# Kernel tuning notes

Hardware: AMD Instinct MI355X
Metric: run time of the kernel (lower is better)

## Reference

```python
import jax, jax.numpy as jnp
import numpy as np

BITS = 4
QMAX = (1 << BITS) - 1      # 15
QHALF = 1 << (BITS - 1)     # 8
B, S = 4, 2048
IN, OUT, FP = 4096, 4096, 256
INT = IN - FP


def setup_inputs() -> dict:
    key = jax.random.key(0)
    k0, k1, k2, k3 = jax.random.split(key, 4)
    x = jax.random.normal(k0, (B, S, IN), dtype=jnp.float16)
    # disjoint outlier / int feature index sets (QUIK splits columns by outlier-ness)
    perm = np.random.default_rng(0).permutation(IN)
    fp_indices = jnp.sort(jnp.asarray(perm[:FP], dtype=jnp.int32))
    int_indices = jnp.sort(jnp.asarray(perm[FP:], dtype=jnp.int32))
    # unpacked int4 weight values in [-8, 7] (torch stores these packed 2-per-uint8)
    int_weight = jax.random.randint(k1, (OUT, INT), -QHALF, QHALF, dtype=jnp.int8)
    weights_scales = (jax.random.uniform(k2, (OUT, 1), dtype=jnp.float32) * 0.01 + 1e-3).astype(jnp.float16)
    fp_weight = (jax.random.normal(k3, (OUT, FP), dtype=jnp.float32) * 0.02).astype(jnp.float16)
    bias = jnp.zeros((OUT,), dtype=jnp.float16)
    # reduced_w[j] = w_scale[j] * sum_k int_weight[j, k]  (precomputed zero-point correction)
    reduced_w = (weights_scales.astype(jnp.float32)[:, 0] * jnp.sum(int_weight.astype(jnp.float32), axis=1)).reshape(1, OUT).astype(jnp.float16)
    return {"x": x, "int_weight": int_weight, "fp_weight": fp_weight, "bias": bias,
            "weights_scales": weights_scales, "reduced_w": reduced_w,
            "int_indices": int_indices, "fp_indices": fp_indices}


def reference(x, int_weight, fp_weight, bias, weights_scales, reduced_w, int_indices, fp_indices):
    b, s, in_feat = x.shape
    xf = x.reshape(-1, in_feat)                       # [N, in] tokens
    int_x = xf[:, int_indices].astype(jnp.float32)    # [N, INT]
    fp_x = xf[:, fp_indices].astype(jnp.float32)      # [N, FP] outliers stay fp16-precision
    # asymmetric per-token quantization (quik.asymmetric.quantize)
    mn = jnp.min(int_x, axis=1, keepdims=True)
    mx = jnp.max(int_x, axis=1, keepdims=True)
    scale = jnp.maximum((mx - mn) / QMAX, 1e-8)       # [N,1]
    q = (jnp.clip(jnp.round((int_x - mn) / scale), 0, QMAX) - QHALF).astype(jnp.int8)  # signed int4 in [-8,7]
    zero = scale * QHALF + mn                         # [N,1] shifted zero point
    # int4 GEMM (quik.matmul.int4Matmul), int32 accumulate
    int_res = jnp.einsum('nk,ok->no', q, int_weight, preferred_element_type=jnp.int32)
    # fp outlier branch fused with bias (F.linear)
    fp_res = fp_x @ fp_weight.astype(jnp.float32).T + bias.astype(jnp.float32)[None, :]
    # quik.asymmetric.dequantize: q*scale_x*scale_w + zero_x*reduced_w + fp_result
    out = (int_res.astype(jnp.float32) * scale * weights_scales.astype(jnp.float32)[:, 0][None, :]
           + zero * reduced_w.astype(jnp.float32) + fp_res)
    return out.astype(jnp.float16).reshape(b, s, -1)
```

## Files before the change

### kernel.cpp

```cpp
#include <hip/hip_runtime.h>
#include <hip/hip_bf16.h>
#include <stdint.h>

#define N_TOK 8192
#define IN_F  4096
#define OUT_F 4096
#define FP_F  256
#define INT_F 3840

typedef int    v4i   __attribute__((ext_vector_type(4)));
typedef int    v16i  __attribute__((ext_vector_type(16)));
typedef float  v16f  __attribute__((ext_vector_type(16)));
typedef __bf16 bf16x8 __attribute__((ext_vector_type(8)));

#define WS_QP   0u
#define WS_WP   31457280u
#define WS_FPX  47185920u
#define WS_WFP  51380224u
#define WS_F1   53477376u
#define WS_F2   53510144u
#define WS_F3   53542912u
#define WS_NEED 53575680u


__global__ __launch_bounds__(256) void zero_out_kernel(uint4* __restrict__ o) {
  o[(size_t)blockIdx.x * 256 + threadIdx.x] = uint4{0, 0, 0, 0};
}

__global__ __launch_bounds__(256, 4) void prep_kernel(
    const float* __restrict__ x,
    const int* __restrict__ int_idx, const int* __restrict__ fp_idx,
    const int* __restrict__ int_w, const float* __restrict__ fp_w,
    uint8_t* __restrict__ qp, uint8_t* __restrict__ wp,
    __hip_bfloat16* __restrict__ fpx, __hip_bfloat16* __restrict__ wfp,
    float* __restrict__ f1, float* __restrict__ f2, float* __restrict__ f3) {
  int tid = threadIdx.x;
  int blk = blockIdx.x;

  if (blk >= 2048) {
    int pb = blk - 2048;
    if (pb < 15360) {
      int t = pb * 256 + tid;
      int r = t / 960, u = t % 960;
      const int* src = int_w + (size_t)r * INT_F + u * 4;
      int4 w4 = *(const int4*)src;
      uint32_t pk = (uint32_t)((w4.x + 8) & 15) |
                    (uint32_t)((w4.y + 8) & 15) << 8 |
                    (uint32_t)((w4.z + 8) & 15) << 16 |
                    (uint32_t)((w4.w + 8) & 15) << 24;
      int g = u >> 2;
      int gp = (g & ~3) | ((g & 3) ^ ((r >> 1) & 3));
      ((uint32_t*)wp)[(size_t)r * 960 + gp * 4 + (u & 3)] = pk;
    } else {
      int t = (pb - 15360) * 256 + tid;
      int i = t * 4;
      int r = i >> 8, c = i & 255;
      float4 v = *(const float4*)(fp_w + i);
      __hip_bfloat16 b[4] = {__float2bfloat16(v.x), __float2bfloat16(v.y),
                             __float2bfloat16(v.z), __float2bfloat16(v.w)};
      int cs = (c & ~0x18) | (((((c) >> 3) & 3) ^ ((r >> 1) & 3)) << 3);
      *(uint2*)(wfp + (size_t)r * 256 + cs) = *(const uint2*)b;
    }
    return;
  }

  int wave = tid >> 6, l = tid & 63;
  int n = blk * 4 + wave;
  const float* xr = x + (size_t)n * IN_F;

  float v[60];
  float lmn = 1e30f, lmx = -1e30f;
#pragma unroll
  for (int k = 0; k < 15; k++) {
    int4 id = *(const int4*)&int_idx[4 * l + 256 * k];
    v[4 * k + 0] = xr[id.x]; v[4 * k + 1] = xr[id.y];
    v[4 * k + 2] = xr[id.z]; v[4 * k + 3] = xr[id.w];
#pragma unroll
    for (int j = 0; j < 4; j++) {
      lmn = fminf(lmn, v[4 * k + j]);
      lmx = fmaxf(lmx, v[4 * k + j]);
    }
  }
  {
    int sw2 = (n >> 1) & 3;
#pragma unroll
    for (int j = 0; j < 4; j++) {
      int c = l + 64 * j;
      int cs = (c & ~0x18) | ((((c >> 3) & 3) ^ sw2) << 3);
      fpx[(size_t)n * FP_F + cs] = __float2bfloat16(xr[fp_idx[c]]);
    }
  }

#pragma unroll
  for (int off = 32; off > 0; off >>= 1) {
    lmn = fminf(lmn, __shfl_xor(lmn, off, 64));
    lmx = fmaxf(lmx, __shfl_xor(lmx, off, 64));
  }
  float mn = lmn;
  float sc = fmaxf((lmx - mn) / 15.0f, 1e-8f);
  float inv = 1.0f / sc;
  if (l == 0) { f1[n] = sc; f3[n] = mn; }

  int sw4 = (n >> 1) & 3;
  uint32_t* qrow = (uint32_t*)(qp + (size_t)n * INT_F);
  float lsum = 0.0f;
#pragma unroll
  for (int k = 0; k < 15; k++) {
    uint32_t pk = 0;
#pragma unroll
    for (int j = 0; j < 4; j++) {
      float c = fminf(fmaxf(rintf((v[4 * k + j] - mn) * inv), 0.0f), 15.0f);
      lsum += c;
      pk |= (uint32_t)c << (8 * j);
    }
    int g = (l >> 2) + 16 * k;
    int gp = (g & ~3) | ((g & 3) ^ sw4);
    qrow[gp * 4 + (l & 3)] = pk;
  }
#pragma unroll
  for (int off = 32; off > 0; off >>= 1) lsum += __shfl_xor(lsum, off, 64);
  if (l == 0) f2[n] = -8.0f * lsum * sc;
}

__device__ __forceinline__ void gl16(const void* g, void* l) {
  __builtin_amdgcn_global_load_lds(
      (const __attribute__((address_space(1))) void*)g,
      (__attribute__((address_space(3))) void*)l, 16, 0, 0);
}

__global__ __launch_bounds__(512, 2) void gemm_kernel(
    const uint8_t* __restrict__ qp, const uint8_t* __restrict__ wp,
    const __hip_bfloat16* __restrict__ fpx, const __hip_bfloat16* __restrict__ wfp,
    const float* __restrict__ f1, const float* __restrict__ f2,
    const float* __restrict__ f3,
    const float* __restrict__ wscale, const float* __restrict__ reduced,
    const float* __restrict__ bias, float* __restrict__ out) {
  __shared__ int4 lds4[6144];
  int8_t* lds = (int8_t*)lds4;

  int tid = threadIdx.x;
  int wave = tid >> 6, lane = tid & 63;
  int wm = wave >> 2, wn = wave & 3;
  int blk = blockIdx.x;
  int wg = (blk & 7) * 64 + (blk >> 3);
  int tileM = wg & 31, tileN = wg >> 5;
  int n0 = tileM * 256, o0 = tileN * 256;

  union { v16i i; v16f f; } acc[4][2];
#pragma unroll
  for (int mi = 0; mi < 4; mi++)
#pragma unroll
    for (int ni = 0; ni < 2; ni++)
#pragma unroll
      for (int e = 0; e < 16; e++) acc[mi][ni].i[e] = 0;

  int m = lane & 31, kg = lane >> 5;

  int row0 = tid >> 2, q16b = (tid & 3) * 16;
  int l0 = tid * 16;
  const uint8_t* gA0 = qp + (size_t)(n0 + row0) * INT_F + q16b;
  const uint8_t* gA1 = qp + (size_t)(n0 + 128 + row0) * INT_F + q16b;
  const uint8_t* gB0 = wp + (size_t)(o0 + row0) * INT_F + q16b;
  const uint8_t* gB1 = wp + (size_t)(o0 + 128 + row0) * INT_F + q16b;

#define STAGE_A(base, kt) do {                                   \
    gl16(gA0 + (kt) * 64, lds + (base) + l0);                    \
    gl16(gA1 + (kt) * 64, lds + (base) + 8192 + l0);             \
  } while (0)
#define STAGE_B(base, kt) do {                                   \
    gl16(gB0 + (kt) * 64, lds + (base) + 16384 + l0);            \
    gl16(gB1 + (kt) * 64, lds + (base) + 24576 + l0);            \
  } while (0)

  STAGE_A(0, 0); STAGE_B(0, 0);
  STAGE_A(32768, 1); STAGE_B(32768, 1);
  asm volatile("s_waitcnt vmcnt(4)" ::: "memory");
  __builtin_amdgcn_s_barrier();

#pragma unroll 1
  for (int t = 0; t < 60; t++) {
    int rb = (t % 3) * 32768;
    int sb = ((t + 2) % 3) * 32768;
    bool st = (t + 2 < 60);
#pragma unroll
    for (int ks = 0; ks < 2; ks++) {
      int s = ks * 2 + kg;
      v4i a[4], b[2];
#pragma unroll
      for (int mi = 0; mi < 4; mi++) {
        int row = wm * 128 + mi * 32 + m;
        a[mi] = *(const v4i*)&lds[rb + row * 64 + ((s ^ ((row >> 1) & 3)) * 16)];
      }
#pragma unroll
      for (int ni = 0; ni < 2; ni++) {
        int row = wn * 64 + ni * 32 + m;
        b[ni] = *(const v4i*)&lds[rb + 16384 + row * 64 + ((s ^ ((row >> 1) & 3)) * 16)];
      }
      if (st) { if (ks == 0) STAGE_A(sb, t + 2); else STAGE_B(sb, t + 2); }
      __builtin_amdgcn_s_barrier();
      asm volatile("s_waitcnt lgkmcnt(0)" ::: "memory");
      __builtin_amdgcn_sched_barrier(0);
      __builtin_amdgcn_s_setprio(1);
#pragma unroll
      for (int mi = 0; mi < 4; mi++)
#pragma unroll
        for (int ni = 0; ni < 2; ni++)
          acc[mi][ni].i = __builtin_amdgcn_mfma_i32_32x32x32_i8(
              a[mi], b[ni], acc[mi][ni].i, 0, 0, 0);
      __builtin_amdgcn_s_setprio(0);
      if (ks == 1) {
        if (t < 58) asm volatile("s_waitcnt vmcnt(4)" ::: "memory");
        else        asm volatile("s_waitcnt vmcnt(0)" ::: "memory");
      }
      __builtin_amdgcn_s_barrier();
    }
  }

  const uint8_t* fxb = (const uint8_t*)fpx;
  const uint8_t* fwb = (const uint8_t*)wfp;
  const uint8_t* gFA0 = fxb + (size_t)(n0 + row0) * 512 + q16b;
  const uint8_t* gFA1 = fxb + (size_t)(n0 + 128 + row0) * 512 + q16b;
  const uint8_t* gFB0 = fwb + (size_t)(o0 + row0) * 512 + q16b;
  const uint8_t* gFB1 = fwb + (size_t)(o0 + 128 + row0) * 512 + q16b;

#define STAGE_FA(base, kr) do {                                  \
    gl16(gFA0 + (kr) * 64, lds + (base) + l0);                   \
    gl16(gFA1 + (kr) * 64, lds + (base) + 8192 + l0);            \
  } while (0)
#define STAGE_FB(base, kr) do {                                  \
    gl16(gFB0 + (kr) * 64, lds + (base) + 16384 + l0);           \
    gl16(gFB1 + (kr) * 64, lds + (base) + 24576 + l0);           \
  } while (0)

  STAGE_FA(0, 0); STAGE_FB(0, 0);

  int col = lane & 31, rb4 = (lane >> 5) * 4;
  float cws[2], crw[2], cbs[2];
#pragma unroll
  for (int ni = 0; ni < 2; ni++) {
    int o = o0 + wn * 64 + ni * 32 + col;
    cws[ni] = wscale[o]; crw[ni] = reduced[o]; cbs[ni] = bias[o];
  }
#pragma unroll
  for (int mi = 0; mi < 4; mi++) {
#pragma unroll
    for (int reg = 0; reg < 16; reg++) {
      int row = (reg & 3) + 8 * (reg >> 2) + rb4;
      int n = n0 + wm * 128 + mi * 32 + row;
      float a1 = f1[n], a2 = f2[n], a3 = f3[n];
      float d0 = (float)acc[mi][0].i[reg];
      float d1 = (float)acc[mi][1].i[reg];
      acc[mi][0].f[reg] = (d0 * a1 + a2) * cws[0] + a3 * crw[0] + cbs[0];
      acc[mi][1].f[reg] = (d1 * a1 + a2) * cws[1] + a3 * crw[1] + cbs[1];
    }
  }
  STAGE_FA(32768, 1); STAGE_FB(32768, 1);
  __builtin_amdgcn_s_barrier();

#pragma unroll 1
  for (int r = 0; r < 8; r++) {
    int rb = (r % 3) * 32768;
    int sb = ((r + 2) % 3) * 32768;
    bool st = (r + 2 < 8);
#pragma unroll
    for (int u = 0; u < 2; u++) {
      int s = u * 2 + kg;
      bf16x8 a[4], b[2];
#pragma unroll
      for (int mi = 0; mi < 4; mi++) {
        int row = wm * 128 + mi * 32 + m;
        a[mi] = *(const bf16x8*)&lds[rb + row * 64 + ((s ^ ((row >> 1) & 3)) * 16)];
      }
#pragma unroll
      for (int ni = 0; ni < 2; ni++) {
        int row = wn * 64 + ni * 32 + m;
        b[ni] = *(const bf16x8*)&lds[rb + 16384 + row * 64 + ((s ^ ((row >> 1) & 3)) * 16)];
      }
      if (st) { if (u == 0) STAGE_FA(sb, r + 2); else STAGE_FB(sb, r + 2); }
      __builtin_amdgcn_s_barrier();
      asm volatile("s_waitcnt lgkmcnt(0)" ::: "memory");
      __builtin_amdgcn_sched_barrier(0);
      __builtin_amdgcn_s_setprio(1);
#pragma unroll
      for (int mi = 0; mi < 4; mi++)
#pragma unroll
        for (int ni = 0; ni < 2; ni++)
          acc[mi][ni].f = __builtin_amdgcn_mfma_f32_32x32x16_bf16(
              a[mi], b[ni], acc[mi][ni].f, 0, 0, 0);
      __builtin_amdgcn_s_setprio(0);
      if (u == 1) {
        if (r < 6) asm volatile("s_waitcnt vmcnt(4)" ::: "memory");
        else       asm volatile("s_waitcnt vmcnt(0)" ::: "memory");
      }
      __builtin_amdgcn_s_barrier();
    }
  }
#undef STAGE_A
#undef STAGE_B
#undef STAGE_FA
#undef STAGE_FB

#pragma unroll
  for (int mi = 0; mi < 4; mi++) {
#pragma unroll
    for (int ni = 0; ni < 2; ni++) {
      int o = o0 + wn * 64 + ni * 32 + col;
#pragma unroll
      for (int reg = 0; reg < 16; reg++) {
        int row = (reg & 3) + 8 * (reg >> 2) + rb4;
        int n = n0 + wm * 128 + mi * 32 + row;
        out[(size_t)n * OUT_F + o] = acc[mi][ni].f[reg];
      }
    }
  }
}

extern "C" void kernel_launch(void* const* d_in, const int* in_sizes, int n_in,
                              void* d_out, int out_size, void* d_ws, size_t ws_size,
                              hipStream_t stream) {
  const float* x     = (const float*)d_in[0];
  const int*   int_w = (const int*)d_in[1];
  const float* fp_w  = (const float*)d_in[2];
  const float* bias  = (const float*)d_in[3];
  const float* wsc   = (const float*)d_in[4];
  const float* red   = (const float*)d_in[5];
  const int*   iidx  = (const int*)d_in[6];
  const int*   fidx  = (const int*)d_in[7];
  float*       out   = (float*)d_out;

  if (ws_size < (size_t)WS_NEED) {
    zero_out_kernel<<<out_size / 1024, 256, 0, stream>>>((uint4*)d_out);
    return;
  }

  uint8_t* ws = (uint8_t*)d_ws;
  uint8_t*        qp  = ws + WS_QP;
  uint8_t*        wpk = ws + WS_WP;
  __hip_bfloat16* fpx = (__hip_bfloat16*)(ws + WS_FPX);
  __hip_bfloat16* wfp = (__hip_bfloat16*)(ws + WS_WFP);
  float*          f1  = (float*)(ws + WS_F1);
  float*          f2  = (float*)(ws + WS_F2);
  float*          f3  = (float*)(ws + WS_F3);

  prep_kernel<<<2048 + 15360 + 1024, 256, 0, stream>>>(
      x, iidx, fidx, int_w, fp_w, qp, wpk, fpx, wfp, f1, f2, f3);
  gemm_kernel<<<(N_TOK / 256) * (OUT_F / 256), 512, 0, stream>>>(
      qp, wpk, fpx, wfp, f1, f2, f3, wsc, red, bias, out);
}
```

Measured before the change: 441.3 us.

## Drop LDS staging; load MFMA fragments directly from k-major packed layout

The prep kernel now writes quantized activations, packed weights and the bf16 outlier operands in a k-slab-major layout, so each wave can fetch its MFMA operand fragments straight from global memory with 16-byte coalesced loads. The GEMM drops shared memory, barriers and global_load_lds staging. It uses 128x128 tiles with 4 waves per block and a three-deep register rotation for software pipelining. This removes LDS traffic and synchronisation, but each wave now re-reads A and B fragments through L2 with no intra-block sharing, and the smaller tiles raise total global traffic.

```diff
diff --git a/kernel.cpp b/kernel.cpp
--- a/kernel.cpp
+++ b/kernel.cpp
@@ -48,9 +48,7 @@
                     (uint32_t)((w4.y + 8) & 15) << 8 |
                     (uint32_t)((w4.z + 8) & 15) << 16 |
                     (uint32_t)((w4.w + 8) & 15) << 24;
-      int g = u >> 2;
-      int gp = (g & ~3) | ((g & 3) ^ ((r >> 1) & 3));
-      ((uint32_t*)wp)[(size_t)r * 960 + gp * 4 + (u & 3)] = pk;
+      *(uint32_t*)(wp + (size_t)(u >> 2) * 65536 + (size_t)r * 16 + (u & 3) * 4) = pk;
     } else {
       int t = (pb - 15360) * 256 + tid;
       int i = t * 4;
@@ -58,8 +56,8 @@
       float4 v = *(const float4*)(fp_w + i);
       __hip_bfloat16 b[4] = {__float2bfloat16(v.x), __float2bfloat16(v.y),
                              __float2bfloat16(v.z), __float2bfloat16(v.w)};
-      int cs = (c & ~0x18) | (((((c) >> 3) & 3) ^ ((r >> 1) & 3)) << 3);
-      *(uint2*)(wfp + (size_t)r * 256 + cs) = *(const uint2*)b;
+      *(uint2*)((uint8_t*)wfp + (size_t)(c >> 3) * 65536 + (size_t)r * 16 + (c & 7) * 2) =
+          *(const uint2*)b;
     }
     return;
   }
@@ -82,13 +80,11 @@
     }
   }
   {
-    int sw2 = (n >> 1) & 3;
-#pragma unroll
-    for (int j = 0; j < 4; j++) {
-      int c = l + 64 * j;
-      int cs = (c & ~0x18) | ((((c >> 3) & 3) ^ sw2) << 3);
-      fpx[(size_t)n * FP_F + cs] = __float2bfloat16(xr[fp_idx[c]]);
-    }
+    int4 fid = *(const int4*)&fp_idx[4 * l];
+    __hip_bfloat16 b[4] = {__float2bfloat16(xr[fid.x]), __float2bfloat16(xr[fid.y]),
+                           __float2bfloat16(xr[fid.z]), __float2bfloat16(xr[fid.w])};
+    *(uint2*)((uint8_t*)fpx + (size_t)(l >> 1) * 131072 + (size_t)n * 16 + (l & 1) * 8) =
+        *(const uint2*)b;
   }
 
 #pragma unroll
@@ -101,8 +97,7 @@
   float inv = 1.0f / sc;
   if (l == 0) { f1[n] = sc; f3[n] = mn; }
 
-  int sw4 = (n >> 1) & 3;
-  uint32_t* qrow = (uint32_t*)(qp + (size_t)n * INT_F);
+  uint8_t* qdst = qp + (size_t)(l >> 2) * 131072 + (size_t)n * 16 + (l & 3) * 4;
   float lsum = 0.0f;
 #pragma unroll
   for (int k = 0; k < 15; k++) {
@@ -113,42 +108,31 @@
       lsum += c;
       pk |= (uint32_t)c << (8 * j);
     }
-    int g = (l >> 2) + 16 * k;
-    int gp = (g & ~3) | ((g & 3) ^ sw4);
-    qrow[gp * 4 + (l & 3)] = pk;
+    *(uint32_t*)(qdst + (size_t)k * 2097152) = pk;
   }
 #pragma unroll
   for (int off = 32; off > 0; off >>= 1) lsum += __shfl_xor(lsum, off, 64);
   if (l == 0) f2[n] = -8.0f * lsum * sc;
 }
 
-__device__ __forceinline__ void gl16(const void* g, void* l) {
-  __builtin_amdgcn_global_load_lds(
-      (const __attribute__((address_space(1))) void*)g,
-      (__attribute__((address_space(3))) void*)l, 16, 0, 0);
-}
-
-__global__ __launch_bounds__(512, 2) void gemm_kernel(
+__global__ __launch_bounds__(256, 3) void gemm_kernel(
     const uint8_t* __restrict__ qp, const uint8_t* __restrict__ wp,
     const __hip_bfloat16* __restrict__ fpx, const __hip_bfloat16* __restrict__ wfp,
     const float* __restrict__ f1, const float* __restrict__ f2,
     const float* __restrict__ f3,
     const float* __restrict__ wscale, const float* __restrict__ reduced,
     const float* __restrict__ bias, float* __restrict__ out) {
-  __shared__ int4 lds4[6144];
-  int8_t* lds = (int8_t*)lds4;
-
   int tid = threadIdx.x;
   int wave = tid >> 6, lane = tid & 63;
-  int wm = wave >> 2, wn = wave & 3;
+  int wm = wave >> 1, wn = wave & 1;
   int blk = blockIdx.x;
-  int wg = (blk & 7) * 64 + (blk >> 3);
-  int tileM = wg & 31, tileN = wg >> 5;
-  int n0 = tileM * 256, o0 = tileN * 256;
-
-  union { v16i i; v16f f; } acc[4][2];
-#pragma unroll
-  for (int mi = 0; mi < 4; mi++)
+  int tileM = ((blk & 7) << 3) | ((blk >> 3) & 7);
+  int tileN = blk >> 6;
+  int n0 = tileM * 128, o0 = tileN * 128;
+
+  union { v16i i; v16f f; } acc[2][2];
+#pragma unroll
+  for (int mi = 0; mi < 2; mi++)
 #pragma unroll
     for (int ni = 0; ni < 2; ni++)
 #pragma unroll
@@ -156,83 +140,56 @@
 
   int m = lane & 31, kg = lane >> 5;
 
-  int row0 = tid >> 2, q16b = (tid & 3) * 16;
-  int l0 = tid * 16;
-  const uint8_t* gA0 = qp + (size_t)(n0 + row0) * INT_F + q16b;
-  const uint8_t* gA1 = qp + (size_t)(n0 + 128 + row0) * INT_F + q16b;
-  const uint8_t* gB0 = wp + (size_t)(o0 + row0) * INT_F + q16b;
-  const uint8_t* gB1 = wp + (size_t)(o0 + 128 + row0) * INT_F + q16b;
-
-#define STAGE_A(base, kt) do {                                   \
-    gl16(gA0 + (kt) * 64, lds + (base) + l0);                    \
-    gl16(gA1 + (kt) * 64, lds + (base) + 8192 + l0);             \
-  } while (0)
-#define STAGE_B(base, kt) do {                                   \
-    gl16(gB0 + (kt) * 64, lds + (base) + 16384 + l0);            \
-    gl16(gB1 + (kt) * 64, lds + (base) + 24576 + l0);            \
-  } while (0)
-
-  STAGE_A(0, 0); STAGE_B(0, 0);
-  STAGE_A(32768, 1); STAGE_B(32768, 1);
-  asm volatile("s_waitcnt vmcnt(4)" ::: "memory");
-  __builtin_amdgcn_s_barrier();
-
+  int offA = kg * 131072 + (n0 + wm * 64 + m) * 16;
+  int offB = kg * 65536  + (o0 + wn * 64 + m) * 16;
+
+#define LOADI(S, s) do {                                          \
+    const uint8_t* pa_ = qp + (size_t)(s) * 262144;               \
+    const uint8_t* pb_ = wp + (size_t)(s) * 131072;               \
+    a0##S = *(const v4i*)(pa_ + offA);                            \
+    a1##S = *(const v4i*)(pa_ + offA + 512);                      \
+    b0##S = *(const v4i*)(pb_ + offB);                            \
+    b1##S = *(const v4i*)(pb_ + offB + 512);                      \
+  } while (0)
+#define MFMAI(S) do {                                                         \
+    acc[0][0].i = __builtin_amdgcn_mfma_i32_32x32x32_i8(a0##S, b0##S, acc[0][0].i, 0, 0, 0); \
+    acc[0][1].i = __builtin_amdgcn_mfma_i32_32x32x32_i8(a0##S, b1##S, acc[0][1].i, 0, 0, 0); \
+    acc[1][0].i = __builtin_amdgcn_mfma_i32_32x32x32_i8(a1##S, b0##S, acc[1][0].i, 0, 0, 0); \
+    acc[1][1].i = __builtin_amdgcn_mfma_i32_32x32x32_i8(a1##S, b1##S, acc[1][1].i, 0, 0, 0); \
+  } while (0)
+
+  {
+    v4i a0A, a1A, b0A, b1A, a0B, a1B, b0B, b1B, a0C, a1C, b0C, b1C;
+    LOADI(A, 0); LOADI(B, 1); LOADI(C, 2);
 #pragma unroll 1
-  for (int t = 0; t < 60; t++) {
-    int rb = (t % 3) * 32768;
-    int sb = ((t + 2) % 3) * 32768;
-    bool st = (t + 2 < 60);
-#pragma unroll
-    for (int ks = 0; ks < 2; ks++) {
-      int s = ks * 2 + kg;
-      v4i a[4], b[2];
-#pragma unroll
-      for (int mi = 0; mi < 4; mi++) {
-        int row = wm * 128 + mi * 32 + m;
-        a[mi] = *(const v4i*)&lds[rb + row * 64 + ((s ^ ((row >> 1) & 3)) * 16)];
-      }
-#pragma unroll
-      for (int ni = 0; ni < 2; ni++) {
-        int row = wn * 64 + ni * 32 + m;
-        b[ni] = *(const v4i*)&lds[rb + 16384 + row * 64 + ((s ^ ((row >> 1) & 3)) * 16)];
-      }
-      if (st) { if (ks == 0) STAGE_A(sb, t + 2); else STAGE_B(sb, t + 2); }
-      __builtin_amdgcn_s_barrier();
-      asm volatile("s_waitcnt lgkmcnt(0)" ::: "memory");
-      __builtin_amdgcn_sched_barrier(0);
-      __builtin_amdgcn_s_setprio(1);
-#pragma unroll
-      for (int mi = 0; mi < 4; mi++)
-#pragma unroll
-        for (int ni = 0; ni < 2; ni++)
-          acc[mi][ni].i = __builtin_amdgcn_mfma_i32_32x32x32_i8(
-              a[mi], b[ni], acc[mi][ni].i, 0, 0, 0);
-      __builtin_amdgcn_s_setprio(0);
-      if (ks == 1) {
-        if (t < 58) asm volatile("s_waitcnt vmcnt(4)" ::: "memory");
-        else        asm volatile("s_waitcnt vmcnt(0)" ::: "memory");
-      }
-      __builtin_amdgcn_s_barrier();
-    }
-  }
+    for (int s = 0; s < 117; s += 3) {
+      MFMAI(A); LOADI(A, s + 3);
+      MFMAI(B); LOADI(B, s + 4);
+      MFMAI(C); LOADI(C, s + 5);
+    }
+    MFMAI(A); MFMAI(B); MFMAI(C);
+  }
+#undef LOADI
 
   const uint8_t* fxb = (const uint8_t*)fpx;
   const uint8_t* fwb = (const uint8_t*)wfp;
-  const uint8_t* gFA0 = fxb + (size_t)(n0 + row0) * 512 + q16b;
-  const uint8_t* gFA1 = fxb + (size_t)(n0 + 128 + row0) * 512 + q16b;
-  const uint8_t* gFB0 = fwb + (size_t)(o0 + row0) * 512 + q16b;
-  const uint8_t* gFB1 = fwb + (size_t)(o0 + 128 + row0) * 512 + q16b;
-
-#define STAGE_FA(base, kr) do {                                  \
-    gl16(gFA0 + (kr) * 64, lds + (base) + l0);                   \
-    gl16(gFA1 + (kr) * 64, lds + (base) + 8192 + l0);            \
-  } while (0)
-#define STAGE_FB(base, kr) do {                                  \
-    gl16(gFB0 + (kr) * 64, lds + (base) + 16384 + l0);           \
-    gl16(gFB1 + (kr) * 64, lds + (base) + 24576 + l0);           \
-  } while (0)
-
-  STAGE_FA(0, 0); STAGE_FB(0, 0);
+#define LOADF(S, s) do {                                          \
+    const uint8_t* pa_ = fxb + (size_t)(s) * 262144;              \
+    const uint8_t* pb_ = fwb + (size_t)(s) * 131072;              \
+    fa0##S = *(const bf16x8*)(pa_ + offA);                        \
+    fa1##S = *(const bf16x8*)(pa_ + offA + 512);                  \
+    fb0##S = *(const bf16x8*)(pb_ + offB);                        \
+    fb1##S = *(const bf16x8*)(pb_ + offB + 512);                  \
+  } while (0)
+#define MFMAF(S) do {                                                         \
+    acc[0][0].f = __builtin_amdgcn_mfma_f32_32x32x16_bf16(fa0##S, fb0##S, acc[0][0].f, 0, 0, 0); \
+    acc[0][1].f = __builtin_amdgcn_mfma_f32_32x32x16_bf16(fa0##S, fb1##S, acc[0][1].f, 0, 0, 0); \
+    acc[1][0].f = __builtin_amdgcn_mfma_f32_32x32x16_bf16(fa1##S, fb0##S, acc[1][0].f, 0, 0, 0); \
+    acc[1][1].f = __builtin_amdgcn_mfma_f32_32x32x16_bf16(fa1##S, fb1##S, acc[1][1].f, 0, 0, 0); \
+  } while (0)
+
+  bf16x8 fa0A, fa1A, fb0A, fb1A, fa0B, fa1B, fb0B, fb1B, fa0C, fa1C, fb0C, fb1C;
+  LOADF(A, 0); LOADF(B, 1); LOADF(C, 2);
 
   int col = lane & 31, rb4 = (lane >> 5) * 4;
   float cws[2], crw[2], cbs[2];
@@ -242,11 +199,11 @@
     cws[ni] = wscale[o]; crw[ni] = reduced[o]; cbs[ni] = bias[o];
   }
 #pragma unroll
-  for (int mi = 0; mi < 4; mi++) {
+  for (int mi = 0; mi < 2; mi++) {
 #pragma unroll
     for (int reg = 0; reg < 16; reg++) {
       int row = (reg & 3) + 8 * (reg >> 2) + rb4;
-      int n = n0 + wm * 128 + mi * 32 + row;
+      int n = n0 + wm * 64 + mi * 32 + row;
       float a1 = f1[n], a2 = f2[n], a3 = f3[n];
       float d0 = (float)acc[mi][0].i[reg];
       float d1 = (float)acc[mi][1].i[reg];
@@ -254,61 +211,27 @@
       acc[mi][1].f[reg] = (d1 * a1 + a2) * cws[1] + a3 * crw[1] + cbs[1];
     }
   }
-  STAGE_FA(32768, 1); STAGE_FB(32768, 1);
-  __builtin_amdgcn_s_barrier();
 
 #pragma unroll 1
-  for (int r = 0; r < 8; r++) {
-    int rb = (r % 3) * 32768;
-    int sb = ((r + 2) % 3) * 32768;
-    bool st = (r + 2 < 8);
-#pragma unroll
-    for (int u = 0; u < 2; u++) {
-      int s = u * 2 + kg;
-      bf16x8 a[4], b[2];
-#pragma unroll
-      for (int mi = 0; mi < 4; mi++) {
-        int row = wm * 128 + mi * 32 + m;
-        a[mi] = *(const bf16x8*)&lds[rb + row * 64 + ((s ^ ((row >> 1) & 3)) * 16)];
-      }
-#pragma unroll
-      for (int ni = 0; ni < 2; ni++) {
-        int row = wn * 64 + ni * 32 + m;
-        b[ni] = *(const bf16x8*)&lds[rb + 16384 + row * 64 + ((s ^ ((row >> 1) & 3)) * 16)];
-      }
-      if (st) { if (u == 0) STAGE_FA(sb, r + 2); else STAGE_FB(sb, r + 2); }
-      __builtin_amdgcn_s_barrier();
-      asm volatile("s_waitcnt lgkmcnt(0)" ::: "memory");
-      __builtin_amdgcn_sched_barrier(0);
-      __builtin_amdgcn_s_setprio(1);
-#pragma unroll
-      for (int mi = 0; mi < 4; mi++)
-#pragma unroll
-        for (int ni = 0; ni < 2; ni++)
-          acc[mi][ni].f = __builtin_amdgcn_mfma_f32_32x32x16_bf16(
-              a[mi], b[ni], acc[mi][ni].f, 0, 0, 0);
-      __builtin_amdgcn_s_setprio(0);
-      if (u == 1) {
-        if (r < 6) asm volatile("s_waitcnt vmcnt(4)" ::: "memory");
-        else       asm volatile("s_waitcnt vmcnt(0)" ::: "memory");
-      }
-      __builtin_amdgcn_s_barrier();
-    }
-  }
-#undef STAGE_A
-#undef STAGE_B
-#undef STAGE_FA
-#undef STAGE_FB
-
-#pragma unroll
-  for (int mi = 0; mi < 4; mi++) {
+  for (int s = 0; s < 15; s += 3) {
+    MFMAF(A); if (s + 3 < 16) LOADF(A, s + 3);
+    MFMAF(B); if (s + 4 < 16) LOADF(B, s + 4);
+    MFMAF(C); if (s + 5 < 16) LOADF(C, s + 5);
+  }
+  MFMAF(A);
+#undef LOADF
+#undef MFMAI
+#undef MFMAF
+
+#pragma unroll
+  for (int mi = 0; mi < 2; mi++) {
 #pragma unroll
     for (int ni = 0; ni < 2; ni++) {
       int o = o0 + wn * 64 + ni * 32 + col;
 #pragma unroll
       for (int reg = 0; reg < 16; reg++) {
         int row = (reg & 3) + 8 * (reg >> 2) + rb4;
-        int n = n0 + wm * 128 + mi * 32 + row;
+        int n = n0 + wm * 64 + mi * 32 + row;
         out[(size_t)n * OUT_F + o] = acc[mi][ni].f[reg];
       }
     }
@@ -344,6 +267,6 @@
 
   prep_kernel<<<2048 + 15360 + 1024, 256, 0, stream>>>(
       x, iidx, fidx, int_w, fp_w, qp, wpk, fpx, wfp, f1, f2, f3);
-  gemm_kernel<<<(N_TOK / 256) * (OUT_F / 256), 512, 0, stream>>>(
+  gemm_kernel<<<(N_TOK / 128) * (OUT_F / 128), 256, 0, stream>>>(
       qp, wpk, fpx, wfp, f1, f2, f3, wsc, red, bias, out);
 }
```

After: 498.4 us. 1.13x slower.
